# Performance work log

Hardware: AMD Instinct MI355X
Metric: run time of the kernel (lower is better)

Reference implementation:

```python
import jax, jax.numpy as jnp
import numpy as np

N_NODES = 50000
N_EDGES = 250000
D_IN, D_HID, D_OUT = 768, 256, 2


def _sage_conv(x, src, dst, W_l, b_l, W_r, n_nodes):
    # PyG SAGEConv (aggr='mean', root_weight=True):
    #   out[i] = lin_l(mean_{j in N(i)} x[j]) + lin_r(x[i])
    msg = x[src]  # [E, d] gather of source-node features
    agg = jax.ops.segment_sum(msg, dst, num_segments=n_nodes)
    cnt = jax.ops.segment_sum(jnp.ones((src.shape[0],), x.dtype), dst,
                              num_segments=n_nodes)
    agg = agg / jnp.maximum(cnt, 1.0)[:, None]
    return agg @ W_l.T + b_l + x @ W_r.T


def setup_inputs() -> dict:
    key = jax.random.key(0)
    ks = jax.random.split(key, 7)
    x = jax.random.normal(ks[0], (N_NODES, D_IN), dtype=jnp.float32)
    edge_index = jax.random.randint(ks[1], (2, N_EDGES), 0, N_NODES,
                                    dtype=jnp.int64)
    s1 = 1.0 / np.sqrt(D_IN)
    s2 = 1.0 / np.sqrt(D_HID)
    W1_l = jax.random.uniform(ks[2], (D_HID, D_IN), jnp.float32, -s1, s1)
    W1_r = jax.random.uniform(ks[3], (D_HID, D_IN), jnp.float32, -s1, s1)
    b1 = jnp.zeros((D_HID,), jnp.float32)
    W2_l = jax.random.uniform(ks[4], (D_OUT, D_HID), jnp.float32, -s2, s2)
    W2_r = jax.random.uniform(ks[5], (D_OUT, D_HID), jnp.float32, -s2, s2)
    b2 = jnp.zeros((D_OUT,), jnp.float32)
    return {"x": x, "edge_index": edge_index,
            "W1_l": W1_l, "b1": b1, "W1_r": W1_r,
            "W2_l": W2_l, "b2": b2, "W2_r": W2_r}


def reference(x, edge_index, W1_l, b1, W1_r, W2_l, b2, W2_r):
    src, dst = edge_index[0], edge_index[1]
    n = x.shape[0]
    h = _sage_conv(x, src, dst, W1_l, b1, W1_r, n)
    h = jax.nn.relu(h)
    # dropout is identity in eval mode (deterministic reference)
    out = _sage_conv(h, src, dst, W2_l, b2, W2_r, n)
    return out
```

## Files before the change

### kernel.cpp

```cpp
#include <hip/hip_runtime.h>
#include <stdint.h>


#define D_IN  768
#define D_HID 256
#define N1    512
#define KITERS (D_IN / 32)

typedef __attribute__((ext_vector_type(8))) short short8;
typedef __attribute__((ext_vector_type(4))) float f32x4;

__device__ __forceinline__ void async_copy16(const void* g, void* l) {
  __builtin_amdgcn_global_load_lds(
      (const __attribute__((address_space(1))) unsigned int*)g,
      (__attribute__((address_space(3))) unsigned int*)l,
      16, 0, 0);
}

__device__ __forceinline__ unsigned short f2bf(float f) {
  union { float f; unsigned u; } v; v.f = f;
  unsigned r = v.u + 0x7FFFu + ((v.u >> 16) & 1u);
  return (unsigned short)(r >> 16);
}

__device__ __forceinline__ float bf2f(unsigned short b) {
  union { unsigned u; float f; } v; v.u = ((unsigned)b) << 16;
  return v.f;
}


__global__ void cvtidx_k(const void* __restrict__ eidx,
                         int* __restrict__ src32, int* __restrict__ dst32,
                         int* __restrict__ counts, int E) {
  __shared__ int flag32;
  int tid = threadIdx.x;
  int i = blockIdx.x * 256 + tid;
  unsigned v = (i < E) ? ((const unsigned int*)eidx)[2 * (size_t)i + 1] : 0u;
  unsigned long long any = __ballot(v != 0u);
  if (tid == 0) flag32 = 0;
  __syncthreads();
  if ((tid & 63) == 0 && any) flag32 = 1;
  __syncthreads();
  if (i >= E) return;
  int s, d;
  if (flag32) {
    const int* p = (const int*)eidx;
    s = p[i]; d = p[E + i];
  } else {
    const long long* p = (const long long*)eidx;
    s = (int)p[i]; d = (int)p[E + i];
  }
  src32[i] = s;
  dst32[i] = d;
  atomicAdd(&counts[d], 1);
}

__global__ void scanA_k(const int* __restrict__ counts,
                        int* __restrict__ blockSums, int M) {
  __shared__ int ts[256];
  int b = blockIdx.x, t = threadIdx.x;
  int base = b * 1024 + t * 4;
  int s = 0;
#pragma unroll
  for (int k = 0; k < 4; k++) { int i = base + k; if (i < M) s += counts[i]; }
  ts[t] = s;
  __syncthreads();
  for (int off = 128; off > 0; off >>= 1) {
    if (t < off) ts[t] += ts[t + off];
    __syncthreads();
  }
  if (t == 0) blockSums[b] = ts[0];
}

__global__ void scanC_k(const int* __restrict__ counts,
                        const int* __restrict__ bsums,
                        int* __restrict__ offs, int* __restrict__ cursor,
                        int M, int E, int nb) {
  __shared__ int ts[256];
  __shared__ int bofs;
  int b = blockIdx.x, t = threadIdx.x;
  if (t < 64) {
    int v = (t < nb) ? bsums[t] : 0;
    int orig = v;
#pragma unroll
    for (int off = 1; off < 64; off <<= 1) {
      int u = __shfl_up(v, off);
      if (t >= off) v += u;
    }
    if (t == b) bofs = v - orig;
  }
  int base = b * 1024 + t * 4;
  int v[4]; int s = 0;
#pragma unroll
  for (int k = 0; k < 4; k++) {
    int i = base + k;
    v[k] = (i < M) ? counts[i] : 0;
    s += v[k];
  }
  ts[t] = s;
  __syncthreads();
  for (int off = 1; off < 256; off <<= 1) {
    int x = (t >= off) ? ts[t - off] : 0;
    __syncthreads();
    ts[t] += x;
    __syncthreads();
  }
  int run = bofs + ts[t] - s;
#pragma unroll
  for (int k = 0; k < 4; k++) {
    int i = base + k;
    if (i < M) { offs[i] = run; cursor[i] = run; run += v[k]; }
  }
  if (b == 0 && t == 0) offs[M] = E;
}

__global__ void fill_k(const int* __restrict__ src, const int* __restrict__ dst,
                       int* __restrict__ cursor, int* __restrict__ csr, int E) {
  int i = blockIdx.x * 256 + threadIdx.x;
  if (i >= E) return;
  int pos = atomicAdd(&cursor[dst[i]], 1);
  csr[pos] = src[i];
}


__global__ void cvtw_k(const float* __restrict__ W1l, const float* __restrict__ W1r,
                       unsigned short* __restrict__ wb) {
  int idx = blockIdx.x * 256 + threadIdx.x;
  int total = N1 * (D_IN / 8);
  if (idx >= total) return;
  int row = idx / (D_IN / 8);
  int cpos = (idx % (D_IN / 8)) * 8;
  const float* p = (row < D_HID) ? (W1l + (size_t)row * D_IN + cpos)
                                 : (W1r + (size_t)(row - D_HID) * D_IN + cpos);
  float4 f0 = *(const float4*)p;
  float4 f1 = *(const float4*)(p + 4);
  short8 o;
  o[0] = (short)f2bf(f0.x); o[1] = (short)f2bf(f0.y);
  o[2] = (short)f2bf(f0.z); o[3] = (short)f2bf(f0.w);
  o[4] = (short)f2bf(f1.x); o[5] = (short)f2bf(f1.y);
  o[6] = (short)f2bf(f1.z); o[7] = (short)f2bf(f1.w);
  *(short8*)(wb + (size_t)idx * 8) = o;
}

__global__ __launch_bounds__(256) void gemm_k(
    const float* __restrict__ x,
    const unsigned short* __restrict__ wb,
    unsigned short* __restrict__ Cb, int M, int MT, int mtPerXcd) {
  __shared__ unsigned short As[2][128 * 32];
  __shared__ unsigned short Bs[3][128 * 32];

  const int bid = blockIdx.x;
  const int xcd = bid & 7;
  const int j   = bid >> 3;
  const int mt  = xcd * mtPerXcd + (j >> 2);
  if (mt >= MT) return;
  const int m0 = mt * 128;
  const int n0 = (j & 3) * 128;

  const int tid  = threadIdx.x;
  const int lane = tid & 63;
  const int wid  = tid >> 6;
  const int wr = wid >> 1, wc = wid & 1;
  const int l15  = lane & 15;
  const int quad = lane >> 4;

  const int arow0 = tid >> 2, akg = tid & 3;
  const int arow1 = arow0 + 64;
  const int aswz = akg | ((akg & 1) << 2);
  const int aoff0 = (arow0 >> 4) * 512 + akg * 128 + ((arow0 & 15) ^ aswz) * 8;
  const int aoff1 = (arow1 >> 4) * 512 + akg * 128 + ((arow1 & 15) ^ aswz) * 8;
  const int pquad = quad | ((quad & 1) << 2);

  const int brow = (tid >> 6) * 16 + (tid & 15);
  const int bcg  = (tid >> 4) & 3;
  const int boff0 = tid * 8;
  const int boff1 = (tid + 256) * 8;

  const float* agp0 = x + (size_t)min(m0 + arow0, M - 1) * D_IN + akg * 8;
  const float* agp1 = x + (size_t)min(m0 + arow1, M - 1) * D_IN + akg * 8;
  const unsigned short* bgp0 = wb + (size_t)(n0 + brow) * D_IN + bcg * 8;
  const unsigned short* bgp1 = wb + (size_t)(n0 + brow + 64) * D_IN + bcg * 8;

  f32x4 acc[4][4];
#pragma unroll
  for (int r = 0; r < 4; r++)
#pragma unroll
    for (int c = 0; c < 4; c++) acc[r][c] = (f32x4)0.0f;

  float4 a0_0, a0_1, a0_2, a0_3;
  float4 a1_0, a1_1, a1_2, a1_3;

  async_copy16(bgp0, &Bs[0][boff0]);
  async_copy16(bgp1, &Bs[0][boff1]);
  asm volatile("" ::: "memory");
  a0_0 = *(const float4*)(agp0);
  a0_1 = *(const float4*)(agp0 + 4);
  a0_2 = *(const float4*)(agp1);
  a0_3 = *(const float4*)(agp1 + 4);
  asm volatile("" ::: "memory");
  async_copy16(bgp0 + 32, &Bs[1][boff0]);
  async_copy16(bgp1 + 32, &Bs[1][boff1]);
  asm volatile("" ::: "memory");
  a1_0 = *(const float4*)(agp0 + 32);
  a1_1 = *(const float4*)(agp0 + 36);
  a1_2 = *(const float4*)(agp1 + 32);
  a1_3 = *(const float4*)(agp1 + 36);

#define GEMM_BODY(P, BR, BW, AR0, AR1, AR2, AR3)                              \
  {                                                                           \
    short8 o0, o1;                                                            \
    o0[0] = (short)f2bf(AR0.x); o0[1] = (short)f2bf(AR0.y);                   \
    o0[2] = (short)f2bf(AR0.z); o0[3] = (short)f2bf(AR0.w);                   \
    o0[4] = (short)f2bf(AR1.x); o0[5] = (short)f2bf(AR1.y);                   \
    o0[6] = (short)f2bf(AR1.z); o0[7] = (short)f2bf(AR1.w);                   \
    o1[0] = (short)f2bf(AR2.x); o1[1] = (short)f2bf(AR2.y);                   \
    o1[2] = (short)f2bf(AR2.z); o1[3] = (short)f2bf(AR2.w);                   \
    o1[4] = (short)f2bf(AR3.x); o1[5] = (short)f2bf(AR3.y);                   \
    o1[6] = (short)f2bf(AR3.z); o1[7] = (short)f2bf(AR3.w);                   \
    *(short8*)&As[P][aoff0] = o0;                                             \
    *(short8*)&As[P][aoff1] = o1;                                             \
    asm volatile("s_waitcnt vmcnt(6) lgkmcnt(0)" ::: "memory");               \
    __builtin_amdgcn_s_barrier();                                             \
    if (kk + 2 < KITERS) {                                                    \
      const int kn = (kk + 2) * 32;                                           \
      async_copy16(bgp0 + kn, &Bs[BW][boff0]);                                \
      async_copy16(bgp1 + kn, &Bs[BW][boff1]);                                \
      asm volatile("" ::: "memory");                                          \
      AR0 = *(const float4*)(agp0 + kn);                                      \
      AR1 = *(const float4*)(agp0 + kn + 4);                                  \
      AR2 = *(const float4*)(agp1 + kn);                                      \
      AR3 = *(const float4*)(agp1 + kn + 4);                                  \
      asm volatile("" ::: "memory");                                          \
    }                                                                         \
    short8 a[4], b[4];                                                        \
    _Pragma("unroll")                                                         \
    for (int r = 0; r < 4; r++)                                               \
      a[r] = *(const short8*)&As[P][(wr * 4 + r) * 512 + quad * 128 +         \
                                    ((l15 ^ pquad)) * 8];                     \
    _Pragma("unroll")                                                         \
    for (int c = 0; c < 4; c++)                                               \
      b[c] = *(const short8*)&Bs[BR][(wc * 4 + c) * 512 + quad * 128 +        \
                                     l15 * 8];                                \
    _Pragma("unroll")                                                         \
    for (int r = 0; r < 4; r++)                                               \
      _Pragma("unroll")                                                       \
      for (int c = 0; c < 4; c++)                                             \
        acc[r][c] =                                                           \
            __builtin_amdgcn_mfma_f32_16x16x32_bf16(a[r], b[c], acc[r][c],    \
                                                    0, 0, 0);                 \
  }

  for (int it = 0; it < KITERS; it += 6) {
    { const int kk = it + 0; GEMM_BODY(0, 0, 2, a0_0, a0_1, a0_2, a0_3) }
    { const int kk = it + 1; GEMM_BODY(1, 1, 0, a1_0, a1_1, a1_2, a1_3) }
    { const int kk = it + 2; GEMM_BODY(0, 2, 1, a0_0, a0_1, a0_2, a0_3) }
    { const int kk = it + 3; GEMM_BODY(1, 0, 2, a1_0, a1_1, a1_2, a1_3) }
    { const int kk = it + 4; GEMM_BODY(0, 1, 0, a0_0, a0_1, a0_2, a0_3) }
    { const int kk = it + 5; GEMM_BODY(1, 2, 1, a1_0, a1_1, a1_2, a1_3) }
  }
#undef GEMM_BODY

  const int crow0 = m0 + wr * 64;
  const int ccol0 = n0 + wc * 64;
#pragma unroll
  for (int r = 0; r < 4; r++)
#pragma unroll
    for (int c = 0; c < 4; c++) {
      int col = ccol0 + c * 16 + l15;
#pragma unroll
      for (int reg = 0; reg < 4; reg++) {
        int row = crow0 + r * 16 + quad * 4 + reg;
        Cb[(size_t)row * N1 + col] = f2bf(acc[r][c][reg]);
      }
    }
}

__global__ void agg_l2_k(const unsigned short* __restrict__ Cb,
                         const int* __restrict__ offs, const int* __restrict__ csr,
                         const float* __restrict__ b1,
                         const float* __restrict__ W2l, const float* __restrict__ W2r,
                         float4* __restrict__ rs, int M) {
  int tid = threadIdx.x;
  int lane = tid & 63;
  int wid = tid >> 6;
  int i = blockIdx.x * 4 + wid;
  if (i >= M) return;
  int c = lane * 4;
  float4 bv  = *(const float4*)(b1 + c);
  float4 wl0 = *(const float4*)(W2l + c);
  float4 wl1 = *(const float4*)(W2l + D_HID + c);
  float4 wr0 = *(const float4*)(W2r + c);
  float4 wr1 = *(const float4*)(W2r + D_HID + c);
  int s = offs[i], e = offs[i + 1];
  ushort4 q = *(const ushort4*)(Cb + (size_t)i * N1 + D_HID + c);
  float ax = 0.f, ay = 0.f, az = 0.f, aw = 0.f;
  float bx = 0.f, by = 0.f, bz = 0.f, bw = 0.f;
  int t = s;
  for (; t + 2 <= e; t += 2) {
    int j0 = csr[t];
    int j1 = csr[t + 1];
    ushort4 v0 = *(const ushort4*)(Cb + (size_t)j0 * N1 + c);
    ushort4 v1 = *(const ushort4*)(Cb + (size_t)j1 * N1 + c);
    ax += bf2f(v0.x); ay += bf2f(v0.y); az += bf2f(v0.z); aw += bf2f(v0.w);
    bx += bf2f(v1.x); by += bf2f(v1.y); bz += bf2f(v1.z); bw += bf2f(v1.w);
  }
  if (t < e) {
    int j = csr[t];
    ushort4 v = *(const ushort4*)(Cb + (size_t)j * N1 + c);
    ax += bf2f(v.x); ay += bf2f(v.y); az += bf2f(v.z); aw += bf2f(v.w);
  }
  ax += bx; ay += by; az += bz; aw += bw;
  float inv = 1.0f / fmaxf((float)(e - s), 1.0f);
  float h0 = fmaxf(ax * inv + bv.x + bf2f(q.x), 0.0f);
  float h1 = fmaxf(ay * inv + bv.y + bf2f(q.y), 0.0f);
  float h2 = fmaxf(az * inv + bv.z + bf2f(q.z), 0.0f);
  float h3 = fmaxf(aw * inv + bv.w + bf2f(q.w), 0.0f);
  float r0 = h0 * wl0.x + h1 * wl0.y + h2 * wl0.z + h3 * wl0.w;
  float r1 = h0 * wl1.x + h1 * wl1.y + h2 * wl1.z + h3 * wl1.w;
  float s0 = h0 * wr0.x + h1 * wr0.y + h2 * wr0.z + h3 * wr0.w;
  float s1 = h0 * wr1.x + h1 * wr1.y + h2 * wr1.z + h3 * wr1.w;
#pragma unroll
  for (int off = 32; off > 0; off >>= 1) {
    r0 += __shfl_xor(r0, off);
    r1 += __shfl_xor(r1, off);
    s0 += __shfl_xor(s0, off);
    s1 += __shfl_xor(s1, off);
  }
  if (lane == 0) rs[i] = make_float4(r0, r1, s0, s1);
}

__global__ void final_k(const float4* __restrict__ rs, const int* __restrict__ offs,
                        const int* __restrict__ csr, const float* __restrict__ b2,
                        float* __restrict__ out, int M) {
  int i = blockIdx.x * 256 + threadIdx.x;
  if (i >= M) return;
  int s = offs[i], e = offs[i + 1];
  float a0 = 0.0f, a1 = 0.0f, b0 = 0.0f, b1 = 0.0f;
  int t = s;
  for (; t + 2 <= e; t += 2) {
    float4 v0 = rs[csr[t]];
    float4 v1 = rs[csr[t + 1]];
    a0 += v0.x; a1 += v0.y;
    b0 += v1.x; b1 += v1.y;
  }
  if (t < e) { float4 v = rs[csr[t]]; a0 += v.x; a1 += v.y; }
  a0 += b0; a1 += b1;
  float inv = 1.0f / fmaxf((float)(e - s), 1.0f);
  float4 me = rs[i];
  out[2 * i + 0] = a0 * inv + b2[0] + me.z;
  out[2 * i + 1] = a1 * inv + b2[1] + me.w;
}


extern "C" void kernel_launch(void* const* d_in, const int* in_sizes, int n_in,
                              void* d_out, int out_size, void* d_ws, size_t ws_size,
                              hipStream_t stream) {
  const float* x   = (const float*)d_in[0];
  const void*  eix = d_in[1];
  const float* W1l = (const float*)d_in[2];
  const float* b1  = (const float*)d_in[3];
  const float* W1r = (const float*)d_in[4];
  const float* W2l = (const float*)d_in[5];
  const float* b2  = (const float*)d_in[6];
  const float* W2r = (const float*)d_in[7];
  float* out = (float*)d_out;

  const int M  = in_sizes[0] / D_IN;
  const int E  = in_sizes[1] / 2;
  const int Mp = ((M + 127) / 128) * 128;
  const int nb = (M + 1023) / 1024;
  const int MT = Mp / 128;
  const int mtPerXcd = (MT + 7) / 8;
  const int gemmBlocks = 8 * mtPerXcd * 4;

  char* ws = (char*)d_ws;
  size_t off = 0;
  auto alloc = [&](size_t b) { size_t o = off; off += (b + 255) & ~(size_t)255; return o; };
  size_t oCounts = alloc((size_t)M * 4);
  size_t zeroBytes = (size_t)M * 4;
  size_t oOffs   = alloc((size_t)(M + 1) * 4);
  size_t oCursor = alloc((size_t)M * 4);
  size_t oCsr    = alloc((size_t)E * 4);
  size_t oSrc    = alloc((size_t)E * 4);
  size_t oDst    = alloc((size_t)E * 4);
  size_t oBSums  = alloc(64 * 4);
  size_t oWb     = alloc((size_t)N1 * D_IN * 2);
  size_t oC      = alloc((size_t)Mp * N1 * 2);
  size_t oRs     = alloc((size_t)M * 16);
  (void)ws_size; (void)n_in; (void)out_size;

  int* counts = (int*)(ws + oCounts);
  int* offs   = (int*)(ws + oOffs);
  int* cursor = (int*)(ws + oCursor);
  int* csr    = (int*)(ws + oCsr);
  int* src32  = (int*)(ws + oSrc);
  int* dst32  = (int*)(ws + oDst);
  int* bsums  = (int*)(ws + oBSums);
  unsigned short* wb = (unsigned short*)(ws + oWb);
  unsigned short* Cb = (unsigned short*)(ws + oC);
  float4* rs = (float4*)(ws + oRs);

  hipMemsetAsync(counts, 0, zeroBytes, stream);

  int gE = (E + 255) / 256;
  cvtidx_k<<<gE, 256, 0, stream>>>(eix, src32, dst32, counts, E);
  scanA_k<<<nb, 256, 0, stream>>>(counts, bsums, M);
  scanC_k<<<nb, 256, 0, stream>>>(counts, bsums, offs, cursor, M, E, nb);
  fill_k<<<gE, 256, 0, stream>>>(src32, dst32, cursor, csr, E);

  int gW = (N1 * (D_IN / 8) + 255) / 256;
  cvtw_k<<<gW, 256, 0, stream>>>(W1l, W1r, wb);

  gemm_k<<<gemmBlocks, 256, 0, stream>>>(x, wb, Cb, M, MT, mtPerXcd);

  agg_l2_k<<<(M + 3) / 4, 256, 0, stream>>>(Cb, offs, csr, b1, W2l, W2r, rs, M);
  final_k<<<(M + 255) / 256, 256, 0, stream>>>(rs, offs, csr, b2, out, M);
}
```

Baseline: 388.7 us.

## Pre-convert x to bf16 in a separate pass and async-load both GEMM operands

Adds a kernel that converts x to bf16 once into a padded workspace buffer. The GEMM then loads A tiles directly into LDS with global_load_lds instead of loading fp32 into registers and converting in the loop. The pipeline is reworked into a double-buffered scheme with two barriers per k-step, and the B buffering drops from three stages to two. The aim is to take conversion work and register pressure out of the GEMM and halve the bytes the GEMM reads for A, which costs an extra full pass over x (fp32 read plus bf16 write). The A LDS layout also loses its XOR swizzle, so fragment reads may hit bank conflicts.

```diff
diff --git a/kernel.cpp b/kernel.cpp
--- a/kernel.cpp
+++ b/kernel.cpp
@@ -142,12 +142,34 @@
   *(short8*)(wb + (size_t)idx * 8) = o;
 }
 
+__global__ void cvtx_k(const float* __restrict__ x,
+                       unsigned short* __restrict__ xb, int M, int Mp) {
+  int idx = blockIdx.x * 256 + threadIdx.x;
+  int total = Mp * (D_IN / 8);
+  if (idx >= total) return;
+  int row = idx / (D_IN / 8);
+  short8 o;
+  if (row < M) {
+    int col = (idx % (D_IN / 8)) * 8;
+    const float* p = x + (size_t)row * D_IN + col;
+    float4 f0 = *(const float4*)p;
+    float4 f1 = *(const float4*)(p + 4);
+    o[0] = (short)f2bf(f0.x); o[1] = (short)f2bf(f0.y);
+    o[2] = (short)f2bf(f0.z); o[3] = (short)f2bf(f0.w);
+    o[4] = (short)f2bf(f1.x); o[5] = (short)f2bf(f1.y);
+    o[6] = (short)f2bf(f1.z); o[7] = (short)f2bf(f1.w);
+  } else {
+    o = (short8)0;
+  }
+  *(short8*)(xb + (size_t)idx * 8) = o;
+}
+
 __global__ __launch_bounds__(256) void gemm_k(
-    const float* __restrict__ x,
+    const unsigned short* __restrict__ xb,
     const unsigned short* __restrict__ wb,
-    unsigned short* __restrict__ Cb, int M, int MT, int mtPerXcd) {
+    unsigned short* __restrict__ Cb, int MT, int mtPerXcd) {
   __shared__ unsigned short As[2][128 * 32];
-  __shared__ unsigned short Bs[3][128 * 32];
+  __shared__ unsigned short Bs[2][128 * 32];
 
   const int bid = blockIdx.x;
   const int xcd = bid & 7;
@@ -165,100 +187,87 @@
   const int quad = lane >> 4;
 
   const int arow0 = tid >> 2, akg = tid & 3;
-  const int arow1 = arow0 + 64;
-  const int aswz = akg | ((akg & 1) << 2);
-  const int aoff0 = (arow0 >> 4) * 512 + akg * 128 + ((arow0 & 15) ^ aswz) * 8;
-  const int aoff1 = (arow1 >> 4) * 512 + akg * 128 + ((arow1 & 15) ^ aswz) * 8;
-  const int pquad = quad | ((quad & 1) << 2);
+  const unsigned short* axp0 = xb + (size_t)(m0 + arow0) * D_IN + akg * 8;
+  const unsigned short* axp1 = xb + (size_t)(m0 + arow0 + 64) * D_IN + akg * 8;
+  const int aoff0 = tid * 8;
+  const int aoff1 = (tid + 256) * 8;
 
   const int brow = (tid >> 6) * 16 + (tid & 15);
   const int bcg  = (tid >> 4) & 3;
+  const unsigned short* bgp0 = wb + (size_t)(n0 + brow) * D_IN + bcg * 8;
+  const unsigned short* bgp1 = wb + (size_t)(n0 + brow + 64) * D_IN + bcg * 8;
   const int boff0 = tid * 8;
   const int boff1 = (tid + 256) * 8;
 
-  const float* agp0 = x + (size_t)min(m0 + arow0, M - 1) * D_IN + akg * 8;
-  const float* agp1 = x + (size_t)min(m0 + arow1, M - 1) * D_IN + akg * 8;
-  const unsigned short* bgp0 = wb + (size_t)(n0 + brow) * D_IN + bcg * 8;
-  const unsigned short* bgp1 = wb + (size_t)(n0 + brow + 64) * D_IN + bcg * 8;
-
   f32x4 acc[4][4];
 #pragma unroll
   for (int r = 0; r < 4; r++)
 #pragma unroll
     for (int c = 0; c < 4; c++) acc[r][c] = (f32x4)0.0f;
 
-  float4 a0_0, a0_1, a0_2, a0_3;
-  float4 a1_0, a1_1, a1_2, a1_3;
-
-  async_copy16(bgp0, &Bs[0][boff0]);
-  async_copy16(bgp1, &Bs[0][boff1]);
-  asm volatile("" ::: "memory");
-  a0_0 = *(const float4*)(agp0);
-  a0_1 = *(const float4*)(agp0 + 4);
-  a0_2 = *(const float4*)(agp1);
-  a0_3 = *(const float4*)(agp1 + 4);
-  asm volatile("" ::: "memory");
-  async_copy16(bgp0 + 32, &Bs[1][boff0]);
-  async_copy16(bgp1 + 32, &Bs[1][boff1]);
-  asm volatile("" ::: "memory");
-  a1_0 = *(const float4*)(agp0 + 32);
-  a1_1 = *(const float4*)(agp0 + 36);
-  a1_2 = *(const float4*)(agp1 + 32);
-  a1_3 = *(const float4*)(agp1 + 36);
-
-#define GEMM_BODY(P, BR, BW, AR0, AR1, AR2, AR3)                              \
+#define STAGE(P, kk)                                                          \
   {                                                                           \
-    short8 o0, o1;                                                            \
-    o0[0] = (short)f2bf(AR0.x); o0[1] = (short)f2bf(AR0.y);                   \
-    o0[2] = (short)f2bf(AR0.z); o0[3] = (short)f2bf(AR0.w);                   \
-    o0[4] = (short)f2bf(AR1.x); o0[5] = (short)f2bf(AR1.y);                   \
-    o0[6] = (short)f2bf(AR1.z); o0[7] = (short)f2bf(AR1.w);                   \
-    o1[0] = (short)f2bf(AR2.x); o1[1] = (short)f2bf(AR2.y);                   \
-    o1[2] = (short)f2bf(AR2.z); o1[3] = (short)f2bf(AR2.w);                   \
-    o1[4] = (short)f2bf(AR3.x); o1[5] = (short)f2bf(AR3.y);                   \
-    o1[6] = (short)f2bf(AR3.z); o1[7] = (short)f2bf(AR3.w);                   \
-    *(short8*)&As[P][aoff0] = o0;                                             \
-    *(short8*)&As[P][aoff1] = o1;                                             \
-    asm volatile("s_waitcnt vmcnt(6) lgkmcnt(0)" ::: "memory");               \
-    __builtin_amdgcn_s_barrier();                                             \
-    if (kk + 2 < KITERS) {                                                    \
-      const int kn = (kk + 2) * 32;                                           \
-      async_copy16(bgp0 + kn, &Bs[BW][boff0]);                                \
-      async_copy16(bgp1 + kn, &Bs[BW][boff1]);                                \
-      asm volatile("" ::: "memory");                                          \
-      AR0 = *(const float4*)(agp0 + kn);                                      \
-      AR1 = *(const float4*)(agp0 + kn + 4);                                  \
-      AR2 = *(const float4*)(agp1 + kn);                                      \
-      AR3 = *(const float4*)(agp1 + kn + 4);                                  \
-      asm volatile("" ::: "memory");                                          \
-    }                                                                         \
-    short8 a[4], b[4];                                                        \
-    _Pragma("unroll")                                                         \
-    for (int r = 0; r < 4; r++)                                               \
-      a[r] = *(const short8*)&As[P][(wr * 4 + r) * 512 + quad * 128 +         \
-                                    ((l15 ^ pquad)) * 8];                     \
+    const int kn = (kk) * 32;                                                 \
+    async_copy16(axp0 + kn, &As[P][aoff0]);                                   \
+    async_copy16(axp1 + kn, &As[P][aoff1]);                                   \
+    async_copy16(bgp0 + kn, &Bs[P][boff0]);                                   \
+    async_copy16(bgp1 + kn, &Bs[P][boff1]);                                   \
+  }
+
+#define READ_FRAGS(P, a, b)                                                   \
+  _Pragma("unroll")                                                           \
+  for (int r = 0; r < 4; r++)                                                 \
+    a[r] = *(const short8*)&As[P][(wr * 64 + r * 16 + l15) * 32 + quad * 8];  \
+  _Pragma("unroll")                                                           \
+  for (int c = 0; c < 4; c++)                                                 \
+    b[c] = *(const short8*)&Bs[P][(wc * 4 + c) * 512 + quad * 128 + l15 * 8];
+
+#define MFMA16(a, b)                                                          \
+  _Pragma("unroll")                                                           \
+  for (int r = 0; r < 4; r++)                                                 \
     _Pragma("unroll")                                                         \
     for (int c = 0; c < 4; c++)                                               \
-      b[c] = *(const short8*)&Bs[BR][(wc * 4 + c) * 512 + quad * 128 +        \
-                                     l15 * 8];                                \
-    _Pragma("unroll")                                                         \
-    for (int r = 0; r < 4; r++)                                               \
-      _Pragma("unroll")                                                       \
-      for (int c = 0; c < 4; c++)                                             \
-        acc[r][c] =                                                           \
-            __builtin_amdgcn_mfma_f32_16x16x32_bf16(a[r], b[c], acc[r][c],    \
-                                                    0, 0, 0);                 \
-  }
-
-  for (int it = 0; it < KITERS; it += 6) {
-    { const int kk = it + 0; GEMM_BODY(0, 0, 2, a0_0, a0_1, a0_2, a0_3) }
-    { const int kk = it + 1; GEMM_BODY(1, 1, 0, a1_0, a1_1, a1_2, a1_3) }
-    { const int kk = it + 2; GEMM_BODY(0, 2, 1, a0_0, a0_1, a0_2, a0_3) }
-    { const int kk = it + 3; GEMM_BODY(1, 0, 2, a1_0, a1_1, a1_2, a1_3) }
-    { const int kk = it + 4; GEMM_BODY(0, 1, 0, a0_0, a0_1, a0_2, a0_3) }
-    { const int kk = it + 5; GEMM_BODY(1, 2, 1, a1_0, a1_1, a1_2, a1_3) }
+      acc[r][c] = __builtin_amdgcn_mfma_f32_16x16x32_bf16(a[r], b[c],         \
+                                                          acc[r][c], 0, 0, 0);
+
+#define GEMM_BODY(P, kk)                                                      \
+  {                                                                           \
+    short8 a[4], b[4];                                                        \
+    READ_FRAGS(P, a, b)                                                       \
+    asm volatile("s_waitcnt lgkmcnt(0)" ::: "memory");                        \
+    __builtin_amdgcn_s_barrier();                                             \
+    STAGE(P, (kk) + 2)                                                        \
+    MFMA16(a, b)                                                              \
+    asm volatile("s_waitcnt vmcnt(4)" ::: "memory");                          \
+    __builtin_amdgcn_s_barrier();                                             \
+  }
+
+  STAGE(0, 0)
+  STAGE(1, 1)
+  asm volatile("s_waitcnt vmcnt(4)" ::: "memory");
+  __builtin_amdgcn_s_barrier();
+
+  for (int it = 0; it < KITERS - 2; it += 2) {
+    GEMM_BODY(0, it)
+    GEMM_BODY(1, it + 1)
+  }
+
+  {
+    short8 a[4], b[4];
+    READ_FRAGS(0, a, b)
+    MFMA16(a, b)
+    asm volatile("s_waitcnt vmcnt(0)" ::: "memory");
+    __builtin_amdgcn_s_barrier();
+  }
+  {
+    short8 a[4], b[4];
+    READ_FRAGS(1, a, b)
+    MFMA16(a, b)
   }
 #undef GEMM_BODY
+#undef MFMA16
+#undef READ_FRAGS
+#undef STAGE
 
   const int crow0 = m0 + wr * 64;
   const int ccol0 = n0 + wc * 64;
@@ -387,6 +396,7 @@
   size_t oWb     = alloc((size_t)N1 * D_IN * 2);
   size_t oC      = alloc((size_t)Mp * N1 * 2);
   size_t oRs     = alloc((size_t)M * 16);
+  size_t oXb     = alloc((size_t)Mp * D_IN * 2);
   (void)ws_size; (void)n_in; (void)out_size;
 
   int* counts = (int*)(ws + oCounts);
@@ -399,6 +409,7 @@
   unsigned short* wb = (unsigned short*)(ws + oWb);
   unsigned short* Cb = (unsigned short*)(ws + oC);
   float4* rs = (float4*)(ws + oRs);
+  unsigned short* xb = (unsigned short*)(ws + oXb);
 
   hipMemsetAsync(counts, 0, zeroBytes, stream);
 
@@ -411,7 +422,10 @@
   int gW = (N1 * (D_IN / 8) + 255) / 256;
   cvtw_k<<<gW, 256, 0, stream>>>(W1l, W1r, wb);
 
-  gemm_k<<<gemmBlocks, 256, 0, stream>>>(x, wb, Cb, M, MT, mtPerXcd);
+  int gX = (Mp * (D_IN / 8) + 255) / 256;
+  cvtx_k<<<gX, 256, 0, stream>>>(x, xb, M, Mp);
+
+  gemm_k<<<gemmBlocks, 256, 0, stream>>>(xb, wb, Cb, MT, mtPerXcd);
 
   agg_l2_k<<<(M + 3) / 4, 256, 0, stream>>>(Cb, offs, csr, b1, W2l, W2r, rs, M);
   final_k<<<(M + 255) / 256, 256, 0, stream>>>(rs, offs, csr, b2, out, M);
```

Result: no change. 387.0 us (-0.4%).
